# Kernel optimization log

Hardware: AMD Instinct MI355X
Metric: run time of the kernel (lower is better)

Reference implementation:

```python
import jax, jax.numpy as jnp
import numpy as np

N_NODES = 50000
N_EDGES = 640000
D_IN = 128
D_H1 = 128
D_H2 = 128
N_CLASSES = 64


def setup_inputs() -> dict:
    key = jax.random.key(0)
    ks = jax.random.split(key, 8)
    x = jax.random.normal(ks[0], (N_NODES, D_IN), dtype=jnp.float32)
    edge_index = jax.random.randint(ks[1], (2, N_EDGES), 0, N_NODES, dtype=jnp.int64)
    s1 = 1.0 / np.sqrt(D_IN)
    s2 = 1.0 / np.sqrt(D_H1)
    s3 = 1.0 / np.sqrt(D_H2)
    W1 = jax.random.uniform(ks[2], (D_IN, D_H1), jnp.float32, -s1, s1)
    b1 = jnp.zeros((D_H1,), jnp.float32)
    W2 = jax.random.uniform(ks[3], (D_H1, D_H2), jnp.float32, -s2, s2)
    b2 = jnp.zeros((D_H2,), jnp.float32)
    Wl = jax.random.uniform(ks[4], (D_H2, N_CLASSES), jnp.float32, -s3, s3)
    bl = jax.random.uniform(ks[5], (N_CLASSES,), jnp.float32, -s3, s3)
    return {"x": x, "edge_index": edge_index, "W1": W1, "b1": b1,
            "W2": W2, "b2": b2, "Wl": Wl, "bl": bl}


def _gcn_norm(edge_index, num_nodes):
    # PyG GCNConv: add self-loops, symmetric normalization D^-1/2 (A+I) D^-1/2
    loop = jnp.arange(num_nodes, dtype=edge_index.dtype)
    src = jnp.concatenate([edge_index[0], loop])
    dst = jnp.concatenate([edge_index[1], loop])
    deg = jax.ops.segment_sum(jnp.ones_like(dst, dtype=jnp.float32), dst,
                              num_segments=num_nodes)
    dinv = jnp.where(deg > 0, jax.lax.rsqrt(deg), 0.0)
    norm = dinv[src] * dinv[dst]  # [E+N]
    return src, dst, norm


def _gcn_conv(h, src, dst, norm, W, b, num_nodes):
    h = h @ W                       # transform first (smaller gather when D_out small)
    msg = h[src] * norm[:, None]    # gather + per-edge scale  [E+N, D_out]
    agg = jax.ops.segment_sum(msg, dst, num_segments=num_nodes)  # scatter-add
    return agg + b


def reference(x, edge_index, W1, b1, W2, b2, Wl, bl):
    n = x.shape[0]
    src, dst, norm = _gcn_norm(edge_index, n)
    h = jax.nn.relu(_gcn_conv(x, src, dst, norm, W1, b1, n))
    # dropout is identity in eval mode
    h = jax.nn.relu(_gcn_conv(h, src, dst, norm, W2, b2, n))
    return h @ Wl + bl
```

## Files before the change

kernel.cpp:

```cpp
#include <hip/hip_runtime.h>


typedef __attribute__((ext_vector_type(8))) __bf16 bf16x8;
typedef __attribute__((ext_vector_type(8))) short short8;
typedef __attribute__((ext_vector_type(4))) float f32x4;
typedef __attribute__((ext_vector_type(2))) float f32x2;

__device__ inline float bf_lo(unsigned u) { return __uint_as_float(u << 16); }
__device__ inline float bf_hi(unsigned u) { return __uint_as_float(u & 0xffff0000u); }
__device__ inline unsigned short f2bf(float v) {
  return __builtin_bit_cast(unsigned short, (__bf16)v);
}
__device__ inline f32x2 pkadd(f32x2 a, f32x2 b) {
  f32x2 d;
  asm("v_pk_add_f32 %0, %1, %2" : "=v"(d) : "v"(a), "v"(b));
  return d;
}
__device__ inline f32x2 bfpair(unsigned w) {
  f32x2 r;
  r.x = __uint_as_float(w << 16);
  r.y = __uint_as_float(w & 0xffff0000u);
  return r;
}

__global__ void k_count_prepW(const int* __restrict__ dst, int E, int nbe,
                              int* __restrict__ cnt, int* __restrict__ rank,
                              const float* __restrict__ W1, const float* __restrict__ W2,
                              const float* __restrict__ Wl,
                              unsigned short* __restrict__ b1h, unsigned short* __restrict__ b1l,
                              unsigned short* __restrict__ b2h, unsigned short* __restrict__ b2l,
                              unsigned short* __restrict__ blh, unsigned short* __restrict__ bll) {
  if ((int)blockIdx.x < nbe) {
    int i = blockIdx.x * 256 + threadIdx.x;
    if (i < E) rank[i] = atomicAdd(&cnt[dst[i]], 1);
  } else {
    int idx = ((int)blockIdx.x - nbe) * 256 + threadIdx.x;
    const float* W;
    unsigned short *bh, *bl_;
    int N, local;
    if (idx < 16384)      { W = W1; bh = b1h; bl_ = b1l; N = 128; local = idx; }
    else if (idx < 32768) { W = W2; bh = b2h; bl_ = b2l; N = 128; local = idx - 16384; }
    else if (idx < 40960) { W = Wl; bh = blh; bl_ = bll; N = 64;  local = idx - 32768; }
    else return;
    int nn = local >> 7, k = local & 127;
    float v = W[(size_t)k * N + nn];
    __bf16 h = (__bf16)v;
    bh[local] = __builtin_bit_cast(unsigned short, h);
    bl_[local] = f2bf(v - (float)h);
  }
}

__global__ void k_scan1(const int* __restrict__ cnt, int n, int* __restrict__ partial,
                        float* __restrict__ dinv) {
  __shared__ int s[256];
  int i = blockIdx.x * 256 + threadIdx.x;
  int v = (i < n) ? cnt[i] : 0;
  s[threadIdx.x] = v;
  if (i < n) dinv[i] = rsqrtf((float)(v + 1));
  __syncthreads();
  for (int off = 128; off > 0; off >>= 1) {
    if (threadIdx.x < off) s[threadIdx.x] += s[threadIdx.x + off];
    __syncthreads();
  }
  if (threadIdx.x == 0) partial[blockIdx.x] = s[0];
}

__global__ void k_scan3(const int* __restrict__ cnt, const int* __restrict__ partial,
                        int nb, int n, int* __restrict__ row_off) {
  __shared__ int s[256];
  __shared__ int base_s;
  int t = threadIdx.x;
  s[t] = (t < nb && t < (int)blockIdx.x) ? partial[t] : 0;
  __syncthreads();
  for (int off = 128; off > 0; off >>= 1) {
    if (t < off) s[t] += s[t + off];
    __syncthreads();
  }
  if (t == 0) base_s = s[0];
  __syncthreads();
  int base = base_s;
  __syncthreads();

  int i = blockIdx.x * 256 + t;
  int v = (i < n) ? cnt[i] : 0;
  s[t] = v;
  __syncthreads();
  for (int off = 1; off < 256; off <<= 1) {
    int u = (t >= off) ? s[t - off] : 0;
    __syncthreads();
    s[t] += u;
    __syncthreads();
  }
  int incl = s[t];
  int excl = incl - v;
  if (i < n) {
    row_off[i] = base + excl;
    if (i == n - 1) row_off[n] = base + incl;
  }
}

__global__ void k_place(const int* __restrict__ src, const int* __restrict__ dst,
                        const int* __restrict__ rank, const int* __restrict__ row_off,
                        int E, unsigned short* __restrict__ edges) {
  int e = blockIdx.x * blockDim.x + threadIdx.x;
  if (e < E) {
    int d = dst[e];
    int pos = row_off[d] + rank[e];
    __builtin_nontemporal_store((unsigned short)src[e], &edges[pos]);
  }
}

template <int NT, bool A32, bool BIAS, bool OUT_BF16, bool SCALE>
__global__ __launch_bounds__(256) void gemm3(
    const void* __restrict__ Ahi_, const unsigned short* __restrict__ Alo,
    const unsigned short* __restrict__ Bhi, const unsigned short* __restrict__ Blo,
    const float* __restrict__ bias, const float* __restrict__ dinv,
    void* __restrict__ Cout, int M) {
  constexpr int K = 128;
  constexpr int NCOL = NT * 16;
  __shared__ alignas(16) unsigned short lbh[NCOL * K];
  __shared__ alignas(16) unsigned short lbl[NCOL * K];
  int t = threadIdx.x;
  int lane = t & 63, wave = t >> 6;
  int lm = lane & 15, lk = lane >> 4;
  int m_base = blockIdx.x * 128 + wave * 32;
  const short8 zero8 = {0, 0, 0, 0, 0, 0, 0, 0};

  if (SCALE && blockIdx.x == 0 && t < 64) {
    *(unsigned*)&((unsigned short*)Cout)[(size_t)M * NCOL + t * 2] = 0u;
  }

  bf16x8 ah[2][4], al[2][4];
  if (A32) {
    const float* Af = (const float*)Ahi_;
    float4 ra[2][4][2];
#pragma unroll
    for (int mt = 0; mt < 2; ++mt) {
      int row = m_base + mt * 16 + lm;
#pragma unroll
      for (int ks = 0; ks < 4; ++ks) {
        if (row < M) {
          ra[mt][ks][0] = *(const float4*)&Af[(size_t)row * K + ks * 32 + lk * 8];
          ra[mt][ks][1] = *(const float4*)&Af[(size_t)row * K + ks * 32 + lk * 8 + 4];
        } else {
          ra[mt][ks][0] = make_float4(0.f, 0.f, 0.f, 0.f);
          ra[mt][ks][1] = make_float4(0.f, 0.f, 0.f, 0.f);
        }
      }
    }
#pragma unroll
    for (int mt = 0; mt < 2; ++mt)
#pragma unroll
      for (int ks = 0; ks < 4; ++ks) {
        float av[8] = {ra[mt][ks][0].x, ra[mt][ks][0].y, ra[mt][ks][0].z, ra[mt][ks][0].w,
                       ra[mt][ks][1].x, ra[mt][ks][1].y, ra[mt][ks][1].z, ra[mt][ks][1].w};
#pragma unroll
        for (int j = 0; j < 8; ++j) {
          __bf16 h = (__bf16)av[j];
          ah[mt][ks][j] = h;
          al[mt][ks][j] = (__bf16)(av[j] - (float)h);
        }
      }
  } else {
    const unsigned short* Ahi = (const unsigned short*)Ahi_;
#pragma unroll
    for (int mt = 0; mt < 2; ++mt) {
      int row = m_base + mt * 16 + lm;
#pragma unroll
      for (int ks = 0; ks < 4; ++ks) {
        if (row < M) {
          ah[mt][ks] = *(const bf16x8*)&Ahi[(size_t)row * K + ks * 32 + lk * 8];
          al[mt][ks] = *(const bf16x8*)&Alo[(size_t)row * K + ks * 32 + lk * 8];
        } else {
          ah[mt][ks] = __builtin_bit_cast(bf16x8, zero8);
          al[mt][ks] = __builtin_bit_cast(bf16x8, zero8);
        }
      }
    }
  }

  for (int c = t; c < NCOL * 16; c += 256) {
    int r = c >> 4, q = c & 15;
    int sq = q ^ (r & 15);
    *(short8*)&lbh[r * K + sq * 8] = *(const short8*)&Bhi[r * K + q * 8];
    *(short8*)&lbl[r * K + sq * 8] = *(const short8*)&Blo[r * K + q * 8];
  }
  __syncthreads();

  f32x4 acc[2][NT] = {};
#pragma unroll
  for (int ks = 0; ks < 4; ++ks) {
    int chunk = ks * 4 + lk;
    bf16x8 bh[NT], bl[NT];
#pragma unroll
    for (int nt = 0; nt < NT; ++nt) {
      int r = nt * 16 + lm;
      int sq = chunk ^ lm;
      bh[nt] = *(const bf16x8*)&lbh[r * K + sq * 8];
      bl[nt] = *(const bf16x8*)&lbl[r * K + sq * 8];
    }
#pragma unroll
    for (int mt = 0; mt < 2; ++mt)
#pragma unroll
      for (int nt = 0; nt < NT; ++nt) {
        acc[mt][nt] = __builtin_amdgcn_mfma_f32_16x16x32_bf16(bh[nt], ah[mt][ks], acc[mt][nt], 0, 0, 0);
        acc[mt][nt] = __builtin_amdgcn_mfma_f32_16x16x32_bf16(bl[nt], ah[mt][ks], acc[mt][nt], 0, 0, 0);
        acc[mt][nt] = __builtin_amdgcn_mfma_f32_16x16x32_bf16(bh[nt], al[mt][ks], acc[mt][nt], 0, 0, 0);
      }
  }

#pragma unroll
  for (int mt = 0; mt < 2; ++mt) {
    int row = m_base + mt * 16 + lm;
    if (row < M) {
      float dr = SCALE ? dinv[row] : 1.f;
#pragma unroll
      for (int nt = 0; nt < NT; ++nt) {
        int col0 = nt * 16 + lk * 4;
        float v0 = acc[mt][nt][0], v1 = acc[mt][nt][1];
        float v2 = acc[mt][nt][2], v3 = acc[mt][nt][3];
        if (SCALE) { v0 *= dr; v1 *= dr; v2 *= dr; v3 *= dr; }
        if (BIAS) {
          float4 bb = *(const float4*)&bias[col0];
          v0 += bb.x; v1 += bb.y; v2 += bb.z; v3 += bb.w;
        }
        if (OUT_BF16) {
          unsigned p0 = (unsigned)f2bf(v0) | ((unsigned)f2bf(v1) << 16);
          unsigned p1 = (unsigned)f2bf(v2) | ((unsigned)f2bf(v3) << 16);
          uint2 pk = make_uint2(p0, p1);
          *(uint2*)&((unsigned short*)Cout)[(size_t)row * NCOL + col0] = pk;
        } else {
          float4 pk = make_float4(v0, v1, v2, v3);
          *(float4*)&((float*)Cout)[(size_t)row * NCOL + col0] = pk;
        }
      }
    }
  }
}

__global__ __launch_bounds__(256) void k_agg(const unsigned short* __restrict__ t,
                      const int* __restrict__ row_off,
                      const unsigned short* __restrict__ edges,
                      const float* __restrict__ dinv, const float* __restrict__ bias,
                      unsigned short* __restrict__ ghi, unsigned short* __restrict__ glo,
                      int n) {
  int wave = threadIdx.x >> 6;
  int lane = threadIdx.x & 63;
  int g = lane >> 4;
  int fl = lane & 15;
  int node = blockIdx.x * 4 + wave;
  if (node >= n) return;
  int2 ro = *(const int2*)&row_off[node];
  int e0 = ro.x, e1 = ro.y;
  int last = e1 - 1;

  float di = dinv[node];
  uint4 sv = *(const uint4*)&t[(size_t)node * 128 + fl * 8];
  float4 bb0 = *(const float4*)&bias[fl * 8];
  float4 bb1 = *(const float4*)&bias[fl * 8 + 4];

  f32x2 acc2[4] = {};
  for (int base = e0; base < e1; base += 16) {
    int i0 = base + g, i1 = i0 + 4, i2 = i0 + 8, i3 = i0 + 12;
    int s0 = edges[i0 < e1 ? i0 : last];
    int s1 = edges[i1 < e1 ? i1 : last];
    int s2 = edges[i2 < e1 ? i2 : last];
    int s3 = edges[i3 < e1 ? i3 : last];
    s0 = i0 < e1 ? s0 : n;
    s1 = i1 < e1 ? s1 : n;
    s2 = i2 < e1 ? s2 : n;
    s3 = i3 < e1 ? s3 : n;
    uint4 u0 = *(const uint4*)&t[(size_t)s0 * 128 + fl * 8];
    uint4 u1 = *(const uint4*)&t[(size_t)s1 * 128 + fl * 8];
    uint4 u2 = *(const uint4*)&t[(size_t)s2 * 128 + fl * 8];
    uint4 u3 = *(const uint4*)&t[(size_t)s3 * 128 + fl * 8];
    acc2[0] = pkadd(acc2[0], pkadd(pkadd(bfpair(u0.x), bfpair(u1.x)),
                                   pkadd(bfpair(u2.x), bfpair(u3.x))));
    acc2[1] = pkadd(acc2[1], pkadd(pkadd(bfpair(u0.y), bfpair(u1.y)),
                                   pkadd(bfpair(u2.y), bfpair(u3.y))));
    acc2[2] = pkadd(acc2[2], pkadd(pkadd(bfpair(u0.z), bfpair(u1.z)),
                                   pkadd(bfpair(u2.z), bfpair(u3.z))));
    acc2[3] = pkadd(acc2[3], pkadd(pkadd(bfpair(u0.w), bfpair(u1.w)),
                                   pkadd(bfpair(u2.w), bfpair(u3.w))));
  }
  float acc[8];
#pragma unroll
  for (int j = 0; j < 4; ++j) { acc[2 * j] = acc2[j].x; acc[2 * j + 1] = acc2[j].y; }
#pragma unroll
  for (int j = 0; j < 8; ++j) {
    acc[j] += __shfl_xor(acc[j], 16);
    acc[j] += __shfl_xor(acc[j], 32);
  }
  if (g == 0) {
    acc[0] += bf_lo(sv.x); acc[1] += bf_hi(sv.x);
    acc[2] += bf_lo(sv.y); acc[3] += bf_hi(sv.y);
    acc[4] += bf_lo(sv.z); acc[5] += bf_hi(sv.z);
    acc[6] += bf_lo(sv.w); acc[7] += bf_hi(sv.w);
    float bb[8] = {bb0.x, bb0.y, bb0.z, bb0.w, bb1.x, bb1.y, bb1.z, bb1.w};
    short8 ho, lo_;
#pragma unroll
    for (int j = 0; j < 8; ++j) {
      float s = fmaxf(acc[j] * di + bb[j], 0.f);
      __bf16 h = (__bf16)s;
      ho[j] = __builtin_bit_cast(short, h);
      lo_[j] = (short)f2bf(s - (float)h);
    }
    *(short8*)&ghi[(size_t)node * 128 + fl * 8] = ho;
    *(short8*)&glo[(size_t)node * 128 + fl * 8] = lo_;
  }
}

extern "C" void kernel_launch(void* const* d_in, const int* in_sizes, int n_in,
                              void* d_out, int out_size, void* d_ws, size_t ws_size,
                              hipStream_t stream) {
  const float* x  = (const float*)d_in[0];
  const int*   ei = (const int*)d_in[1];
  const float* W1 = (const float*)d_in[2];
  const float* b1 = (const float*)d_in[3];
  const float* W2 = (const float*)d_in[4];
  const float* b2 = (const float*)d_in[5];
  const float* Wl = (const float*)d_in[6];
  const float* bl = (const float*)d_in[7];
  float* out = (float*)d_out;

  const int D = 128;
  int N = in_sizes[0] / D;
  int E = in_sizes[1] / 2;
  const int* src = ei;
  const int* dst = ei + E;

  uintptr_t ws = (uintptr_t)d_ws;
  auto take = [&](size_t bytes) {
    uintptr_t p = ws;
    ws += (bytes + 15) & ~(size_t)15;
    return p;
  };
  unsigned short* t_bf = (unsigned short*)take(((size_t)N + 1) * D * 2);
  unsigned short* xh   = (unsigned short*)take((size_t)N * D * 2);
  unsigned short* xl   = (unsigned short*)take((size_t)N * D * 2);
  unsigned short* edges = (unsigned short*)take((size_t)E * 2);
  int*   rank    = (int*)take((size_t)E * 4);
  int*   cnt     = (int*)take((size_t)N * sizeof(int));
  int*   row_off = (int*)take(((size_t)N + 1) * sizeof(int));
  float* dinv    = (float*)take((size_t)N * sizeof(float));
  int*   partial = (int*)take(256 * sizeof(int));
  unsigned short* b1h = (unsigned short*)take(128 * 128 * 2);
  unsigned short* b1l = (unsigned short*)take(128 * 128 * 2);
  unsigned short* b2h = (unsigned short*)take(128 * 128 * 2);
  unsigned short* b2l = (unsigned short*)take(128 * 128 * 2);
  unsigned short* blh = (unsigned short*)take(128 * 64 * 2);
  unsigned short* bll = (unsigned short*)take(128 * 64 * 2);

  int nb_n = (N + 255) / 256;
  int nb_e = (E + 255) / 256;

  hipMemsetAsync(cnt, 0, (size_t)N * sizeof(int), stream);
  k_count_prepW<<<nb_e + 160, 256, 0, stream>>>(dst, E, nb_e, cnt, rank,
                                                W1, W2, Wl, b1h, b1l, b2h, b2l, blh, bll);
  k_scan1<<<nb_n, 256, 0, stream>>>(cnt, N, partial, dinv);
  k_scan3<<<nb_n, 256, 0, stream>>>(cnt, partial, nb_n, N, row_off);
  k_place<<<nb_e, 256, 0, stream>>>(src, dst, rank, row_off, E, edges);

  int gemm_blocks = (N + 127) / 128;
  int agg_blocks = (N + 3) / 4;

  gemm3<8, true, false, true, true><<<gemm_blocks, 256, 0, stream>>>(
      x, nullptr, b1h, b1l, nullptr, dinv, t_bf, N);
  k_agg<<<agg_blocks, 256, 0, stream>>>(t_bf, row_off, edges, dinv, b1, xh, xl, N);
  gemm3<8, false, false, true, true><<<gemm_blocks, 256, 0, stream>>>(
      xh, xl, b2h, b2l, nullptr, dinv, t_bf, N);
  k_agg<<<agg_blocks, 256, 0, stream>>>(t_bf, row_off, edges, dinv, b2, xh, xl, N);
  gemm3<4, false, true, false, false><<<gemm_blocks, 256, 0, stream>>>(
      xh, xl, blh, bll, bl, nullptr, out, N);
}
```

Measured before the change: 228.9 us.

## Split feature matrices into 32-column planes for cache-local gather aggregation

Stores intermediate bf16 feature matrices as four column-planar slices of 32 features and makes each aggregation block handle one slice for eight nodes, with eight lanes per edge group. The GEMM kernels read and write the planar layout. The intent is to shrink the gather working set per slice so neighbor rows stay in cache, at the cost of smaller 64-byte gather segments and more blocks.

```diff
diff --git a/kernel.cpp b/kernel.cpp
--- a/kernel.cpp
+++ b/kernel.cpp
@@ -120,6 +120,7 @@
   constexpr int NCOL = NT * 16;
   __shared__ alignas(16) unsigned short lbh[NCOL * K];
   __shared__ alignas(16) unsigned short lbl[NCOL * K];
+  const size_t P = (size_t)(M + 1) * 32;
   int t = threadIdx.x;
   int lane = t & 63, wave = t >> 6;
   int lm = lane & 15, lk = lane >> 4;
@@ -127,7 +128,7 @@
   const short8 zero8 = {0, 0, 0, 0, 0, 0, 0, 0};
 
   if (SCALE && blockIdx.x == 0 && t < 64) {
-    *(unsigned*)&((unsigned short*)Cout)[(size_t)M * NCOL + t * 2] = 0u;
+    *(unsigned*)&((unsigned short*)Cout)[(size_t)(t >> 4) * P + (size_t)M * 32 + (t & 15) * 2] = 0u;
   }
 
   bf16x8 ah[2][4], al[2][4];
@@ -169,8 +170,8 @@
 #pragma unroll
       for (int ks = 0; ks < 4; ++ks) {
         if (row < M) {
-          ah[mt][ks] = *(const bf16x8*)&Ahi[(size_t)row * K + ks * 32 + lk * 8];
-          al[mt][ks] = *(const bf16x8*)&Alo[(size_t)row * K + ks * 32 + lk * 8];
+          ah[mt][ks] = *(const bf16x8*)&Ahi[(size_t)ks * P + (size_t)row * 32 + lk * 8];
+          al[mt][ks] = *(const bf16x8*)&Alo[(size_t)ks * P + (size_t)row * 32 + lk * 8];
         } else {
           ah[mt][ks] = __builtin_bit_cast(bf16x8, zero8);
           al[mt][ks] = __builtin_bit_cast(bf16x8, zero8);
@@ -228,7 +229,7 @@
           unsigned p0 = (unsigned)f2bf(v0) | ((unsigned)f2bf(v1) << 16);
           unsigned p1 = (unsigned)f2bf(v2) | ((unsigned)f2bf(v3) << 16);
           uint2 pk = make_uint2(p0, p1);
-          *(uint2*)&((unsigned short*)Cout)[(size_t)row * NCOL + col0] = pk;
+          *(uint2*)&((unsigned short*)Cout)[(size_t)(col0 >> 5) * P + (size_t)row * 32 + (col0 & 31)] = pk;
         } else {
           float4 pk = make_float4(v0, v1, v2, v3);
           *(float4*)&((float*)Cout)[(size_t)row * NCOL + col0] = pk;
@@ -244,52 +245,48 @@
                       const float* __restrict__ dinv, const float* __restrict__ bias,
                       unsigned short* __restrict__ ghi, unsigned short* __restrict__ glo,
                       int n) {
+  const size_t P = (size_t)(n + 1) * 32;
+  int q = blockIdx.x & 3;
   int wave = threadIdx.x >> 6;
   int lane = threadIdx.x & 63;
-  int g = lane >> 4;
-  int fl = lane & 15;
-  int node = blockIdx.x * 4 + wave;
+  int nh = lane >> 5;
+  int r = lane & 31;
+  int g = r >> 2;
+  int fl = r & 3;
+  int node = (blockIdx.x >> 2) * 8 + wave * 2 + nh;
   if (node >= n) return;
   int2 ro = *(const int2*)&row_off[node];
   int e0 = ro.x, e1 = ro.y;
   int last = e1 - 1;
 
+  const unsigned short* tq = t + (size_t)q * P;
   float di = dinv[node];
-  uint4 sv = *(const uint4*)&t[(size_t)node * 128 + fl * 8];
-  float4 bb0 = *(const float4*)&bias[fl * 8];
-  float4 bb1 = *(const float4*)&bias[fl * 8 + 4];
+  uint4 sv = *(const uint4*)&tq[(size_t)node * 32 + fl * 8];
+  float4 bb0 = *(const float4*)&bias[q * 32 + fl * 8];
+  float4 bb1 = *(const float4*)&bias[q * 32 + fl * 8 + 4];
 
   f32x2 acc2[4] = {};
   for (int base = e0; base < e1; base += 16) {
-    int i0 = base + g, i1 = i0 + 4, i2 = i0 + 8, i3 = i0 + 12;
+    int i0 = base + g, i1 = base + 8 + g;
     int s0 = edges[i0 < e1 ? i0 : last];
     int s1 = edges[i1 < e1 ? i1 : last];
-    int s2 = edges[i2 < e1 ? i2 : last];
-    int s3 = edges[i3 < e1 ? i3 : last];
     s0 = i0 < e1 ? s0 : n;
     s1 = i1 < e1 ? s1 : n;
-    s2 = i2 < e1 ? s2 : n;
-    s3 = i3 < e1 ? s3 : n;
-    uint4 u0 = *(const uint4*)&t[(size_t)s0 * 128 + fl * 8];
-    uint4 u1 = *(const uint4*)&t[(size_t)s1 * 128 + fl * 8];
-    uint4 u2 = *(const uint4*)&t[(size_t)s2 * 128 + fl * 8];
-    uint4 u3 = *(const uint4*)&t[(size_t)s3 * 128 + fl * 8];
-    acc2[0] = pkadd(acc2[0], pkadd(pkadd(bfpair(u0.x), bfpair(u1.x)),
-                                   pkadd(bfpair(u2.x), bfpair(u3.x))));
-    acc2[1] = pkadd(acc2[1], pkadd(pkadd(bfpair(u0.y), bfpair(u1.y)),
-                                   pkadd(bfpair(u2.y), bfpair(u3.y))));
-    acc2[2] = pkadd(acc2[2], pkadd(pkadd(bfpair(u0.z), bfpair(u1.z)),
-                                   pkadd(bfpair(u2.z), bfpair(u3.z))));
-    acc2[3] = pkadd(acc2[3], pkadd(pkadd(bfpair(u0.w), bfpair(u1.w)),
-                                   pkadd(bfpair(u2.w), bfpair(u3.w))));
+    uint4 u0 = *(const uint4*)&tq[(size_t)s0 * 32 + fl * 8];
+    uint4 u1 = *(const uint4*)&tq[(size_t)s1 * 32 + fl * 8];
+    acc2[0] = pkadd(acc2[0], pkadd(bfpair(u0.x), bfpair(u1.x)));
+    acc2[1] = pkadd(acc2[1], pkadd(bfpair(u0.y), bfpair(u1.y)));
+    acc2[2] = pkadd(acc2[2], pkadd(bfpair(u0.z), bfpair(u1.z)));
+    acc2[3] = pkadd(acc2[3], pkadd(bfpair(u0.w), bfpair(u1.w)));
   }
   float acc[8];
 #pragma unroll
   for (int j = 0; j < 4; ++j) { acc[2 * j] = acc2[j].x; acc[2 * j + 1] = acc2[j].y; }
 #pragma unroll
   for (int j = 0; j < 8; ++j) {
+    acc[j] += __shfl_xor(acc[j], 4);
+    acc[j] += __shfl_xor(acc[j], 8);
     acc[j] += __shfl_xor(acc[j], 16);
-    acc[j] += __shfl_xor(acc[j], 32);
   }
   if (g == 0) {
     acc[0] += bf_lo(sv.x); acc[1] += bf_hi(sv.x);
@@ -305,8 +302,8 @@
       ho[j] = __builtin_bit_cast(short, h);
       lo_[j] = (short)f2bf(s - (float)h);
     }
-    *(short8*)&ghi[(size_t)node * 128 + fl * 8] = ho;
-    *(short8*)&glo[(size_t)node * 128 + fl * 8] = lo_;
+    *(short8*)&ghi[(size_t)q * P + (size_t)node * 32 + fl * 8] = ho;
+    *(short8*)&glo[(size_t)q * P + (size_t)node * 32 + fl * 8] = lo_;
   }
 }
 
@@ -336,8 +333,8 @@
     return p;
   };
   unsigned short* t_bf = (unsigned short*)take(((size_t)N + 1) * D * 2);
-  unsigned short* xh   = (unsigned short*)take((size_t)N * D * 2);
-  unsigned short* xl   = (unsigned short*)take((size_t)N * D * 2);
+  unsigned short* xh   = (unsigned short*)take(((size_t)N + 1) * D * 2);
+  unsigned short* xl   = (unsigned short*)take(((size_t)N + 1) * D * 2);
   unsigned short* edges = (unsigned short*)take((size_t)E * 2);
   int*   rank    = (int*)take((size_t)E * 4);
   int*   cnt     = (int*)take((size_t)N * sizeof(int));
@@ -362,7 +359,7 @@
   k_place<<<nb_e, 256, 0, stream>>>(src, dst, rank, row_off, E, edges);
 
   int gemm_blocks = (N + 127) / 128;
-  int agg_blocks = (N + 3) / 4;
+  int agg_blocks = 4 * ((N + 7) / 8);
 
   gemm3<8, true, false, true, true><<<gemm_blocks, 256, 0, stream>>>(
       x, nullptr, b1h, b1l, nullptr, dinv, t_bf, N);
```

Measured after the change: 251.5 us. 1.1x slower.

## Pad CSR rows to multiples of 16 and emit fp32 aggregation output

Applied to the files above, without the earlier changes.

Each row in the CSR is padded to a multiple of 16 entries, and the padding is pre-filled with a sentinel index that points at a zero row, so the aggregation loop no longer needs bounds checks or selects on edge indices. The aggregation kernel now writes fp32 output directly, and the following GEMMs split it into bf16 hi/lo on the fly instead of reading precomputed hi/lo arrays. The cost is extra padded edge traversal (up to 15 wasted gathers of the zero row per node), a fill pass over the enlarged edge buffer, and fp32 writes and reads of the intermediate.

```diff
diff --git a/kernel.cpp b/kernel.cpp
--- a/kernel.cpp
+++ b/kernel.cpp
@@ -23,8 +23,9 @@
   return r;
 }
 
-__global__ void k_count_prepW(const int* __restrict__ dst, int E, int nbe,
+__global__ void k_count_prepW(const int* __restrict__ dst, int E, int nbe, int n,
                               int* __restrict__ cnt, int* __restrict__ rank,
+                              unsigned short* __restrict__ edges, int fill_q,
                               const float* __restrict__ W1, const float* __restrict__ W2,
                               const float* __restrict__ Wl,
                               unsigned short* __restrict__ b1h, unsigned short* __restrict__ b1l,
@@ -33,7 +34,7 @@
   if ((int)blockIdx.x < nbe) {
     int i = blockIdx.x * 256 + threadIdx.x;
     if (i < E) rank[i] = atomicAdd(&cnt[dst[i]], 1);
-  } else {
+  } else if ((int)blockIdx.x < nbe + 160) {
     int idx = ((int)blockIdx.x - nbe) * 256 + threadIdx.x;
     const float* W;
     unsigned short *bh, *bl_;
@@ -47,6 +48,12 @@
     __bf16 h = (__bf16)v;
     bh[local] = __builtin_bit_cast(unsigned short, h);
     bl_[local] = f2bf(v - (float)h);
+  } else {
+    int b = (int)blockIdx.x - nbe - 160;
+    unsigned w = ((unsigned)n << 16) | (unsigned)n;
+    uint4 val = make_uint4(w, w, w, w);
+    for (int i = b * 256 + threadIdx.x; i < fill_q; i += 64 * 256)
+      ((uint4*)edges)[i] = val;
   }
 }
 
@@ -55,7 +62,7 @@
   __shared__ int s[256];
   int i = blockIdx.x * 256 + threadIdx.x;
   int v = (i < n) ? cnt[i] : 0;
-  s[threadIdx.x] = v;
+  s[threadIdx.x] = (v + 15) & ~15;
   if (i < n) dinv[i] = rsqrtf((float)(v + 1));
   __syncthreads();
   for (int off = 128; off > 0; off >>= 1) {
@@ -82,7 +89,7 @@
   __syncthreads();
 
   int i = blockIdx.x * 256 + t;
-  int v = (i < n) ? cnt[i] : 0;
+  int v = (i < n) ? ((cnt[i] + 15) & ~15) : 0;
   s[t] = v;
   __syncthreads();
   for (int off = 1; off < 256; off <<= 1) {
@@ -242,8 +249,7 @@
                       const int* __restrict__ row_off,
                       const unsigned short* __restrict__ edges,
                       const float* __restrict__ dinv, const float* __restrict__ bias,
-                      unsigned short* __restrict__ ghi, unsigned short* __restrict__ glo,
-                      int n) {
+                      float* __restrict__ gout, int n) {
   int wave = threadIdx.x >> 6;
   int lane = threadIdx.x & 63;
   int g = lane >> 4;
@@ -252,7 +258,6 @@
   if (node >= n) return;
   int2 ro = *(const int2*)&row_off[node];
   int e0 = ro.x, e1 = ro.y;
-  int last = e1 - 1;
 
   float di = dinv[node];
   uint4 sv = *(const uint4*)&t[(size_t)node * 128 + fl * 8];
@@ -261,15 +266,10 @@
 
   f32x2 acc2[4] = {};
   for (int base = e0; base < e1; base += 16) {
-    int i0 = base + g, i1 = i0 + 4, i2 = i0 + 8, i3 = i0 + 12;
-    int s0 = edges[i0 < e1 ? i0 : last];
-    int s1 = edges[i1 < e1 ? i1 : last];
-    int s2 = edges[i2 < e1 ? i2 : last];
-    int s3 = edges[i3 < e1 ? i3 : last];
-    s0 = i0 < e1 ? s0 : n;
-    s1 = i1 < e1 ? s1 : n;
-    s2 = i2 < e1 ? s2 : n;
-    s3 = i3 < e1 ? s3 : n;
+    int s0 = edges[base + g];
+    int s1 = edges[base + 4 + g];
+    int s2 = edges[base + 8 + g];
+    int s3 = edges[base + 12 + g];
     uint4 u0 = *(const uint4*)&t[(size_t)s0 * 128 + fl * 8];
     uint4 u1 = *(const uint4*)&t[(size_t)s1 * 128 + fl * 8];
     uint4 u2 = *(const uint4*)&t[(size_t)s2 * 128 + fl * 8];
@@ -297,16 +297,17 @@
     acc[4] += bf_lo(sv.z); acc[5] += bf_hi(sv.z);
     acc[6] += bf_lo(sv.w); acc[7] += bf_hi(sv.w);
     float bb[8] = {bb0.x, bb0.y, bb0.z, bb0.w, bb1.x, bb1.y, bb1.z, bb1.w};
-    short8 ho, lo_;
-#pragma unroll
-    for (int j = 0; j < 8; ++j) {
-      float s = fmaxf(acc[j] * di + bb[j], 0.f);
-      __bf16 h = (__bf16)s;
-      ho[j] = __builtin_bit_cast(short, h);
-      lo_[j] = (short)f2bf(s - (float)h);
-    }
-    *(short8*)&ghi[(size_t)node * 128 + fl * 8] = ho;
-    *(short8*)&glo[(size_t)node * 128 + fl * 8] = lo_;
+    float4 o0, o1;
+    o0.x = fmaxf(acc[0] * di + bb[0], 0.f);
+    o0.y = fmaxf(acc[1] * di + bb[1], 0.f);
+    o0.z = fmaxf(acc[2] * di + bb[2], 0.f);
+    o0.w = fmaxf(acc[3] * di + bb[3], 0.f);
+    o1.x = fmaxf(acc[4] * di + bb[4], 0.f);
+    o1.y = fmaxf(acc[5] * di + bb[5], 0.f);
+    o1.z = fmaxf(acc[6] * di + bb[6], 0.f);
+    o1.w = fmaxf(acc[7] * di + bb[7], 0.f);
+    *(float4*)&gout[(size_t)node * 128 + fl * 8] = o0;
+    *(float4*)&gout[(size_t)node * 128 + fl * 8 + 4] = o1;
   }
 }
 
@@ -335,10 +336,10 @@
     ws += (bytes + 15) & ~(size_t)15;
     return p;
   };
+  size_t Epad = (size_t)E + 16 * (size_t)N + 8;
   unsigned short* t_bf = (unsigned short*)take(((size_t)N + 1) * D * 2);
-  unsigned short* xh   = (unsigned short*)take((size_t)N * D * 2);
-  unsigned short* xl   = (unsigned short*)take((size_t)N * D * 2);
-  unsigned short* edges = (unsigned short*)take((size_t)E * 2);
+  float* xf            = (float*)take((size_t)N * D * 4);
+  unsigned short* edges = (unsigned short*)take(Epad * 2);
   int*   rank    = (int*)take((size_t)E * 4);
   int*   cnt     = (int*)take((size_t)N * sizeof(int));
   int*   row_off = (int*)take(((size_t)N + 1) * sizeof(int));
@@ -353,10 +354,12 @@
 
   int nb_n = (N + 255) / 256;
   int nb_e = (E + 255) / 256;
+  int fill_q = (int)(Epad / 8);
 
   hipMemsetAsync(cnt, 0, (size_t)N * sizeof(int), stream);
-  k_count_prepW<<<nb_e + 160, 256, 0, stream>>>(dst, E, nb_e, cnt, rank,
-                                                W1, W2, Wl, b1h, b1l, b2h, b2l, blh, bll);
+  k_count_prepW<<<nb_e + 160 + 64, 256, 0, stream>>>(dst, E, nb_e, N, cnt, rank,
+                                                     edges, fill_q,
+                                                     W1, W2, Wl, b1h, b1l, b2h, b2l, blh, bll);
   k_scan1<<<nb_n, 256, 0, stream>>>(cnt, N, partial, dinv);
   k_scan3<<<nb_n, 256, 0, stream>>>(cnt, partial, nb_n, N, row_off);
   k_place<<<nb_e, 256, 0, stream>>>(src, dst, rank, row_off, E, edges);
@@ -366,10 +369,10 @@
 
   gemm3<8, true, false, true, true><<<gemm_blocks, 256, 0, stream>>>(
       x, nullptr, b1h, b1l, nullptr, dinv, t_bf, N);
-  k_agg<<<agg_blocks, 256, 0, stream>>>(t_bf, row_off, edges, dinv, b1, xh, xl, N);
-  gemm3<8, false, false, true, true><<<gemm_blocks, 256, 0, stream>>>(
-      xh, xl, b2h, b2l, nullptr, dinv, t_bf, N);
-  k_agg<<<agg_blocks, 256, 0, stream>>>(t_bf, row_off, edges, dinv, b2, xh, xl, N);
-  gemm3<4, false, true, false, false><<<gemm_blocks, 256, 0, stream>>>(
-      xh, xl, blh, bll, bl, nullptr, out, N);
-}
+  k_agg<<<agg_blocks, 256, 0, stream>>>(t_bf, row_off, edges, dinv, b1, xf, N);
+  gemm3<8, true, false, true, true><<<gemm_blocks, 256, 0, stream>>>(
+      xf, nullptr, b2h, b2l, nullptr, dinv, t_bf, N);
+  k_agg<<<agg_blocks, 256, 0, stream>>>(t_bf, row_off, edges, dinv, b2, xf, N);
+  gemm3<4, true, true, false, false><<<gemm_blocks, 256, 0, stream>>>(
+      xf, nullptr, blh, bll, bl, nullptr, out, N);
+}
```

Result: no change. 232.2 us (+1.4%).
